# Kernel tuning notes

Hardware: AMD Instinct MI355X
Metric: run time of the kernel (lower is better)

The kernel has to match this reference:

```python
import jax, jax.numpy as jnp
import numpy as np

NUM_EXPERT = 8
TOP_K = 1


def setup_inputs() -> dict:
    key = jax.random.key(0)
    ks = jax.random.split(key, 6)
    B, S, D, E, F = 8, 2048, 768, 8, 469
    scale = 0.02
    return {
        "x": jax.random.normal(ks[0], (B, S, D), dtype=jnp.float32),
        "Wg": jax.random.normal(ks[1], (E, D), dtype=jnp.float32) * scale,
        "bg": jnp.zeros((E,), dtype=jnp.float32),
        "W1": jax.random.normal(ks[2], (E, F, D), dtype=jnp.float32) * scale,
        "W2": jax.random.normal(ks[3], (E, F, D), dtype=jnp.float32) * scale,
        "W3": jax.random.normal(ks[4], (E, D, F), dtype=jnp.float32) * scale,
    }


def reference(x, Wg, bg, W1, W2, W3):
    # x: [B, S, D]; Wg: [E, D]; W1/W2: [E, F, D] (torch Linear layout [out,in]); W3: [E, D, F]
    B, S, D = x.shape
    E = Wg.shape[0]
    xf = x.reshape(B * S, D)  # [T, D]

    # gating: top-k over expert logits, softmax over the selected logits
    gate = xf @ Wg.T + bg  # [T, E]
    vals, idx = jax.lax.top_k(gate, TOP_K)  # [T, K]
    probs = jax.nn.softmax(vals, axis=-1)  # [T, K] (all ones for K=1)

    # combine weights per (token, expert): sum over k slots of onehot * prob
    dispatch = jnp.sum(
        jax.nn.one_hot(idx, E, dtype=x.dtype) * probs[..., None], axis=1
    )  # [T, E]

    # dense grouped SwiGLU FFN over all experts, combined by dispatch weights
    h = jax.nn.silu(jnp.einsum("td,efd->tef", xf, W1)) * jnp.einsum(
        "td,efd->tef", xf, W2
    )  # [T, E, F]
    out = jnp.einsum("tef,edf,te->td", h, W3, dispatch)  # [T, D]
    return out.reshape(B, S, D)
```

## Files before the change

kernel.cpp:

```cpp
#include <hip/hip_runtime.h>
#include <hip/hip_bf16.h>
#include <stdint.h>

#define TT 16384
#define DD 768
#define EE 8
#define FF 469
#define FP 512
#define NCHUNK (TT / 64)
#define MAXT 71

typedef __attribute__((ext_vector_type(8))) short s16x8;
typedef __attribute__((ext_vector_type(4))) float f32x4;

__device__ __forceinline__ ushort f2bf(float f) {
  uint32_t u = __builtin_bit_cast(uint32_t, f);
  u += 0x7fffu + ((u >> 16) & 1u);
  return (ushort)(u >> 16);
}

__device__ __forceinline__ void gload16(const void* g, void* l) {
  __builtin_amdgcn_global_load_lds((const __attribute__((address_space(1))) unsigned int*)g,
                                   (__attribute__((address_space(3))) unsigned int*)l,
                                   16, 0, 0);
}

#define N12 (EE * 2 * FP * (DD / 4))
#define N3  (EE * DD * (FP / 4))
__global__ __launch_bounds__(256) void prep_kernel(
    const float* __restrict__ x, const float* __restrict__ Wg,
    const float* __restrict__ bg, const float* __restrict__ W1,
    const float* __restrict__ W2, const float* __restrict__ W3,
    int* __restrict__ eidx, ushort* __restrict__ xbf, int* __restrict__ cnt,
    ushort* __restrict__ w12b, ushort* __restrict__ w3b) {
  int tid = threadIdx.x;
  if (blockIdx.x < TT / 4) {
    __shared__ float4 wgs[EE * DD / 4];
    for (int i = tid; i < EE * DD / 4; i += 256) wgs[i] = ((const float4*)Wg)[i];
    __syncthreads();

    int t = blockIdx.x * 4 + (tid >> 6);
    int lane = tid & 63;
    const float4* xr = (const float4*)(x + (size_t)t * DD);
    float4 xv[3];
#pragma unroll
    for (int k = 0; k < 3; ++k) xv[k] = xr[lane + 64 * k];

    float acc[EE];
#pragma unroll
    for (int e = 0; e < EE; ++e) acc[e] = 0.f;
#pragma unroll
    for (int k = 0; k < 3; ++k) {
#pragma unroll
      for (int e = 0; e < EE; ++e) {
        float4 w = wgs[e * 192 + lane + 64 * k];
        acc[e] += xv[k].x * w.x + xv[k].y * w.y + xv[k].z * w.z + xv[k].w * w.w;
      }
    }

    uint2* xd = (uint2*)(xbf + (size_t)t * DD);
#pragma unroll
    for (int k = 0; k < 3; ++k) {
      union { ushort u[4]; uint2 w; } p;
      p.u[0] = f2bf(xv[k].x); p.u[1] = f2bf(xv[k].y);
      p.u[2] = f2bf(xv[k].z); p.u[3] = f2bf(xv[k].w);
      xd[lane + 64 * k] = p.w;
    }

#pragma unroll
    for (int off = 32; off; off >>= 1) {
#pragma unroll
      for (int e = 0; e < EE; ++e) acc[e] += __shfl_down(acc[e], off);
    }
    if (lane == 0) {
      float best = acc[0] + bg[0];
      int bi = 0;
#pragma unroll
      for (int e = 1; e < EE; ++e) {
        float v = acc[e] + bg[e];
        if (v > best) { best = v; bi = e; }
      }
      eidx[t] = bi;
      atomicAdd(&cnt[bi * NCHUNK + (t >> 6)], 1);
    }
  } else {
    int vb = blockIdx.x - TT / 4;
    for (int i = vb * 256 + tid; i < N12 + N3; i += 2048 * 256) {
      if (i < N12) {
        int d4 = i % (DD / 4);
        int er = i / (DD / 4);
        int row = er & 1023;
        int e = er >> 10;
        int f = row >> 1;
        union { ushort u[4]; uint2 w; } p;
        if (f < FF) {
          const float* src = ((row & 1) ? W2 : W1) + ((size_t)e * FF + f) * DD;
          float4 v = ((const float4*)src)[d4];
          p.u[0] = f2bf(v.x); p.u[1] = f2bf(v.y); p.u[2] = f2bf(v.z); p.u[3] = f2bf(v.w);
        } else {
          p.w.x = 0u; p.w.y = 0u;
        }
        ((uint2*)w12b)[i] = p.w;
      } else {
        int j = i - N12;
        int f4 = (j % (FP / 4)) * 4;
        int ed = j / (FP / 4);
        union { ushort u[4]; uint2 w; } p;
#pragma unroll
        for (int q = 0; q < 4; ++q) {
          int f = f4 + q;
          p.u[q] = (f < FF) ? f2bf(W3[(size_t)ed * FF + f]) : (ushort)0;
        }
        ((uint2*)w3b)[(size_t)ed * (FP / 4) + (f4 >> 2)] = p.w;
      }
    }
  }
}

__global__ void scan_kernel(const int* __restrict__ cnt, int* __restrict__ scanEx,
                            int* __restrict__ offs, int* __restrict__ tileE,
                            int* __restrict__ tileT0) {
  int e = threadIdx.x >> 6;
  int lane = threadIdx.x & 63;
  __shared__ int totals[EE];
  int carry = 0;
#pragma unroll
  for (int g = 0; g < NCHUNK / 64; ++g) {
    int v = cnt[e * NCHUNK + g * 64 + lane];
    int s = v;
#pragma unroll
    for (int d = 1; d < 64; d <<= 1) {
      int t = __shfl_up(s, d);
      if (lane >= d) s += t;
    }
    scanEx[e * NCHUNK + g * 64 + lane] = carry + s - v;
    carry += __shfl(s, 63);
  }
  if (lane == 0) totals[e] = carry;
  __syncthreads();
  if (threadIdx.x == 0) {
    int s = 0;
    for (int e2 = 0; e2 < EE; ++e2) { offs[e2] = s; s += totals[e2]; }
    offs[EE] = s;
    int idx = 0;
    for (int e2 = 0; e2 < EE; ++e2) {
      int nt = (totals[e2] + 255) >> 8;
      for (int j = 0; j < nt; ++j) { tileE[idx] = e2; tileT0[idx] = j << 8; ++idx; }
    }
    for (; idx < MAXT; ++idx) tileE[idx] = -1;
  }
}

__global__ void scatter2_kernel(const int* __restrict__ eidx, const int* __restrict__ offs,
                                const int* __restrict__ scanEx, int* __restrict__ perm) {
  int c = blockIdx.x * 4 + (threadIdx.x >> 6);
  int lane = threadIdx.x & 63;
  int t = c * 64 + lane;
  int v = eidx[t];
  unsigned long long mym = 0;
#pragma unroll
  for (int e = 0; e < EE; ++e) {
    unsigned long long me = __ballot(v == e);
    if (v == e) mym = me;
  }
  int rank = __popcll(mym & ((1ULL << lane) - 1ULL));
  perm[offs[v] + scanEx[v * NCHUNK + c] + rank] = t;
}

__global__ __launch_bounds__(512, 2) void ffn1_kernel(
    const ushort* __restrict__ xbf, const ushort* __restrict__ w12b,
    const int* __restrict__ perm, const int* __restrict__ offs,
    const int* __restrict__ tileE, const int* __restrict__ tileT0,
    ushort* __restrict__ hbf) {
  int bid = blockIdx.x;
  int xcd = bid & 7, idx = bid >> 3;
  int L = (xcd < 4) ? xcd * 36 + idx : 144 + (xcd - 4) * 35 + idx;
  int ti = L >> 2, y = L & 3;
  int e = tileE[ti];
  if (e < 0) return;
  int tile0 = tileT0[ti];
  int gOff = offs[e];
  int Ne = offs[e + 1] - gOff;
  int n0 = y * 256;

  __shared__ __align__(16) short As[2][256 * 64];
  __shared__ __align__(16) short Bs[2][256 * 64];

  int tid = threadIdx.x;
  int w = tid >> 6, lane = tid & 63;
  int l8 = lane >> 3, lg = lane & 7;
  int gsrc = (lg ^ l8) * 8;

  int last = gOff + Ne - 1;
  const ushort* aSrc[4];
  const ushort* bSrc[4];
#pragma unroll
  for (int j = 0; j < 4; ++j) {
    int row = w * 32 + j * 8 + l8;
    int tok = perm[min(gOff + tile0 + row, last)];
    aSrc[j] = xbf + (size_t)tok * DD + gsrc;
    bSrc[j] = w12b + ((size_t)(e << 10) + n0 + row) * DD + gsrc;
  }
  int sdst[4];
#pragma unroll
  for (int j = 0; j < 4; ++j) sdst[j] = (w * 32 + j * 8) * 64;

  int wr = w >> 2, wc = w & 3;
  int lrow = lane & 15, kh = lane >> 4;
  int sw0 = (kh ^ (lrow & 7)) * 8;
  int sw1 = ((4 + kh) ^ (lrow & 7)) * 8;
  int aBase = (wr * 128 + lrow) * 64;
  int bBase = (wc * 64 + lrow) * 64;

  f32x4 acc[2][2][4][2];
#pragma unroll
  for (int mh = 0; mh < 2; ++mh)
#pragma unroll
    for (int nh = 0; nh < 2; ++nh)
#pragma unroll
      for (int mm = 0; mm < 4; ++mm)
#pragma unroll
        for (int nn = 0; nn < 2; ++nn)
          acc[mh][nh][mm][nn] = (f32x4){0.f, 0.f, 0.f, 0.f};

#pragma unroll
  for (int j = 0; j < 4; ++j) gload16(aSrc[j], &As[0][sdst[j]]);
#pragma unroll
  for (int j = 0; j < 4; ++j) gload16(bSrc[j], &Bs[0][sdst[j]]);

  const int NT = DD / 64;
#pragma unroll
  for (int kt = 0; kt < NT; ++kt) {
    const int s = kt & 1;
    asm volatile("s_waitcnt vmcnt(0)" ::: "memory");
    __builtin_amdgcn_s_barrier();
    __builtin_amdgcn_sched_barrier(0);
    const int ko = (kt + 1) * 64;
    const bool more = (kt + 1 < NT);

    s16x8 a[4][2], b[2][2][2];
    if (more) {
      gload16(aSrc[0] + ko, &As[s ^ 1][sdst[0]]);
      gload16(aSrc[1] + ko, &As[s ^ 1][sdst[1]]);
    }
#pragma unroll
    for (int nh = 0; nh < 2; ++nh)
#pragma unroll
      for (int nn = 0; nn < 2; ++nn) {
        int rb = bBase + (nh * 32 + nn * 16) * 64;
        b[nh][nn][0] = *(const s16x8*)&Bs[s][rb + sw0];
        b[nh][nn][1] = *(const s16x8*)&Bs[s][rb + sw1];
      }
#pragma unroll
    for (int mm = 0; mm < 4; ++mm) {
      int ra = aBase + (mm * 16) * 64;
      a[mm][0] = *(const s16x8*)&As[s][ra + sw0];
      a[mm][1] = *(const s16x8*)&As[s][ra + sw1];
    }
    __builtin_amdgcn_s_setprio(1);
#pragma unroll
    for (int mm = 0; mm < 4; ++mm)
#pragma unroll
      for (int nn = 0; nn < 2; ++nn)
#pragma unroll
        for (int ks = 0; ks < 2; ++ks)
          acc[0][0][mm][nn] = __builtin_amdgcn_mfma_f32_16x16x32_bf16(a[mm][ks], b[0][nn][ks], acc[0][0][mm][nn], 0, 0, 0);
    __builtin_amdgcn_s_setprio(0);
    if (more) {
      gload16(aSrc[2] + ko, &As[s ^ 1][sdst[2]]);
      gload16(aSrc[3] + ko, &As[s ^ 1][sdst[3]]);
    }
    __builtin_amdgcn_s_setprio(1);
#pragma unroll
    for (int mm = 0; mm < 4; ++mm)
#pragma unroll
      for (int nn = 0; nn < 2; ++nn)
#pragma unroll
        for (int ks = 0; ks < 2; ++ks)
          acc[0][1][mm][nn] = __builtin_amdgcn_mfma_f32_16x16x32_bf16(a[mm][ks], b[1][nn][ks], acc[0][1][mm][nn], 0, 0, 0);
    __builtin_amdgcn_s_setprio(0);
    if (more) {
      gload16(bSrc[0] + ko, &Bs[s ^ 1][sdst[0]]);
      gload16(bSrc[1] + ko, &Bs[s ^ 1][sdst[1]]);
    }
#pragma unroll
    for (int mm = 0; mm < 4; ++mm) {
      int ra = aBase + (64 + mm * 16) * 64;
      a[mm][0] = *(const s16x8*)&As[s][ra + sw0];
      a[mm][1] = *(const s16x8*)&As[s][ra + sw1];
    }
    __builtin_amdgcn_s_setprio(1);
#pragma unroll
    for (int mm = 0; mm < 4; ++mm)
#pragma unroll
      for (int nn = 0; nn < 2; ++nn)
#pragma unroll
        for (int ks = 0; ks < 2; ++ks)
          acc[1][0][mm][nn] = __builtin_amdgcn_mfma_f32_16x16x32_bf16(a[mm][ks], b[0][nn][ks], acc[1][0][mm][nn], 0, 0, 0);
    __builtin_amdgcn_s_setprio(0);
    if (more) {
      gload16(bSrc[2] + ko, &Bs[s ^ 1][sdst[2]]);
      gload16(bSrc[3] + ko, &Bs[s ^ 1][sdst[3]]);
    }
    __builtin_amdgcn_s_setprio(1);
#pragma unroll
    for (int mm = 0; mm < 4; ++mm)
#pragma unroll
      for (int nn = 0; nn < 2; ++nn)
#pragma unroll
        for (int ks = 0; ks < 2; ++ks)
          acc[1][1][mm][nn] = __builtin_amdgcn_mfma_f32_16x16x32_bf16(a[mm][ks], b[1][nn][ks], acc[1][1][mm][nn], 0, 0, 0);
    __builtin_amdgcn_s_setprio(0);
  }

#pragma unroll
  for (int mh = 0; mh < 2; ++mh)
#pragma unroll
    for (int nh = 0; nh < 2; ++nh)
#pragma unroll
      for (int mm = 0; mm < 4; ++mm)
#pragma unroll
        for (int nn = 0; nn < 2; ++nn) {
          int f = (n0 + wc * 64 + nh * 32 + nn * 16 + lrow) >> 1;
          int rbase = tile0 + wr * 128 + mh * 64 + mm * 16 + kh * 4;
#pragma unroll
          for (int r = 0; r < 4; ++r) {
            float val = acc[mh][nh][mm][nn][r];
            float par = __shfl_xor(val, 1);
            float u = (lane & 1) ? par : val;
            float vv = (lane & 1) ? val : par;
            float h = (u / (1.f + __expf(-u))) * vv;
            int gr = rbase + r;
            if (!(lane & 1) && gr < Ne)
              hbf[(size_t)(gOff + gr) * FP + f] = f2bf(h);
          }
        }
}

__global__ __launch_bounds__(512, 2) void ffn2_kernel(
    const ushort* __restrict__ hbf, const ushort* __restrict__ w3b,
    const int* __restrict__ perm, const int* __restrict__ offs,
    const int* __restrict__ tileE, const int* __restrict__ tileT0,
    float* __restrict__ out) {
  int bid = blockIdx.x;
  int xcd = bid & 7, idx = bid >> 3;
  int L = (xcd < 5) ? xcd * 27 + idx : 135 + (xcd - 5) * 26 + idx;
  int ti = L / 3, y = L % 3;
  int e = tileE[ti];
  if (e < 0) return;
  int tile0 = tileT0[ti];
  int gOff = offs[e];
  int Ne = offs[e + 1] - gOff;
  int d0 = y * 256;

  __shared__ __align__(16) short As[2][256 * 64];
  __shared__ __align__(16) short Bs[2][256 * 64];

  int tid = threadIdx.x;
  int w = tid >> 6, lane = tid & 63;
  int l8 = lane >> 3, lg = lane & 7;
  int gsrc = (lg ^ l8) * 8;

  int last = gOff + Ne - 1;
  const ushort* aSrc[4];
  const ushort* bSrc[4];
#pragma unroll
  for (int j = 0; j < 4; ++j) {
    int row = w * 32 + j * 8 + l8;
    aSrc[j] = hbf + (size_t)min(gOff + tile0 + row, last) * FP + gsrc;
    bSrc[j] = w3b + ((size_t)e * DD + d0 + row) * FP + gsrc;
  }
  int sdst[4];
#pragma unroll
  for (int j = 0; j < 4; ++j) sdst[j] = (w * 32 + j * 8) * 64;

  int wr = w >> 2, wc = w & 3;
  int lrow = lane & 15, kh = lane >> 4;
  int sw0 = (kh ^ (lrow & 7)) * 8;
  int sw1 = ((4 + kh) ^ (lrow & 7)) * 8;
  int aBase = (wr * 128 + lrow) * 64;
  int bBase = (wc * 64 + lrow) * 64;

  f32x4 acc[2][2][4][2];
#pragma unroll
  for (int mh = 0; mh < 2; ++mh)
#pragma unroll
    for (int nh = 0; nh < 2; ++nh)
#pragma unroll
      for (int mm = 0; mm < 4; ++mm)
#pragma unroll
        for (int nn = 0; nn < 2; ++nn)
          acc[mh][nh][mm][nn] = (f32x4){0.f, 0.f, 0.f, 0.f};

#pragma unroll
  for (int j = 0; j < 4; ++j) gload16(aSrc[j], &As[0][sdst[j]]);
#pragma unroll
  for (int j = 0; j < 4; ++j) gload16(bSrc[j], &Bs[0][sdst[j]]);

  const int NT = FP / 64;
#pragma unroll
  for (int kt = 0; kt < NT; ++kt) {
    const int s = kt & 1;
    asm volatile("s_waitcnt vmcnt(0)" ::: "memory");
    __builtin_amdgcn_s_barrier();
    __builtin_amdgcn_sched_barrier(0);
    const int ko = (kt + 1) * 64;
    const bool more = (kt + 1 < NT);

    s16x8 a[4][2], b[2][2][2];
    if (more) {
      gload16(aSrc[0] + ko, &As[s ^ 1][sdst[0]]);
      gload16(aSrc[1] + ko, &As[s ^ 1][sdst[1]]);
    }
#pragma unroll
    for (int nh = 0; nh < 2; ++nh)
#pragma unroll
      for (int nn = 0; nn < 2; ++nn) {
        int rb = bBase + (nh * 32 + nn * 16) * 64;
        b[nh][nn][0] = *(const s16x8*)&Bs[s][rb + sw0];
        b[nh][nn][1] = *(const s16x8*)&Bs[s][rb + sw1];
      }
#pragma unroll
    for (int mm = 0; mm < 4; ++mm) {
      int ra = aBase + (mm * 16) * 64;
      a[mm][0] = *(const s16x8*)&As[s][ra + sw0];
      a[mm][1] = *(const s16x8*)&As[s][ra + sw1];
    }
    __builtin_amdgcn_s_setprio(1);
#pragma unroll
    for (int mm = 0; mm < 4; ++mm)
#pragma unroll
      for (int nn = 0; nn < 2; ++nn)
#pragma unroll
        for (int ks = 0; ks < 2; ++ks)
          acc[0][0][mm][nn] = __builtin_amdgcn_mfma_f32_16x16x32_bf16(a[mm][ks], b[0][nn][ks], acc[0][0][mm][nn], 0, 0, 0);
    __builtin_amdgcn_s_setprio(0);
    if (more) {
      gload16(aSrc[2] + ko, &As[s ^ 1][sdst[2]]);
      gload16(aSrc[3] + ko, &As[s ^ 1][sdst[3]]);
    }
    __builtin_amdgcn_s_setprio(1);
#pragma unroll
    for (int mm = 0; mm < 4; ++mm)
#pragma unroll
      for (int nn = 0; nn < 2; ++nn)
#pragma unroll
        for (int ks = 0; ks < 2; ++ks)
          acc[0][1][mm][nn] = __builtin_amdgcn_mfma_f32_16x16x32_bf16(a[mm][ks], b[1][nn][ks], acc[0][1][mm][nn], 0, 0, 0);
    __builtin_amdgcn_s_setprio(0);
    if (more) {
      gload16(bSrc[0] + ko, &Bs[s ^ 1][sdst[0]]);
      gload16(bSrc[1] + ko, &Bs[s ^ 1][sdst[1]]);
    }
#pragma unroll
    for (int mm = 0; mm < 4; ++mm) {
      int ra = aBase + (64 + mm * 16) * 64;
      a[mm][0] = *(const s16x8*)&As[s][ra + sw0];
      a[mm][1] = *(const s16x8*)&As[s][ra + sw1];
    }
    __builtin_amdgcn_s_setprio(1);
#pragma unroll
    for (int mm = 0; mm < 4; ++mm)
#pragma unroll
      for (int nn = 0; nn < 2; ++nn)
#pragma unroll
        for (int ks = 0; ks < 2; ++ks)
          acc[1][0][mm][nn] = __builtin_amdgcn_mfma_f32_16x16x32_bf16(a[mm][ks], b[0][nn][ks], acc[1][0][mm][nn], 0, 0, 0);
    __builtin_amdgcn_s_setprio(0);
    if (more) {
      gload16(bSrc[2] + ko, &Bs[s ^ 1][sdst[2]]);
      gload16(bSrc[3] + ko, &Bs[s ^ 1][sdst[3]]);
    }
    __builtin_amdgcn_s_setprio(1);
#pragma unroll
    for (int mm = 0; mm < 4; ++mm)
#pragma unroll
      for (int nn = 0; nn < 2; ++nn)
#pragma unroll
        for (int ks = 0; ks < 2; ++ks)
          acc[1][1][mm][nn] = __builtin_amdgcn_mfma_f32_16x16x32_bf16(a[mm][ks], b[1][nn][ks], acc[1][1][mm][nn], 0, 0, 0);
    __builtin_amdgcn_s_setprio(0);
  }

#pragma unroll
  for (int mh = 0; mh < 2; ++mh)
#pragma unroll
    for (int nh = 0; nh < 2; ++nh)
#pragma unroll
      for (int mm = 0; mm < 4; ++mm)
#pragma unroll
        for (int nn = 0; nn < 2; ++nn) {
          int col = d0 + wc * 64 + nh * 32 + nn * 16 + lrow;
          int rbase = tile0 + wr * 128 + mh * 64 + mm * 16 + kh * 4;
#pragma unroll
          for (int r = 0; r < 4; ++r) {
            int gr = rbase + r;
            if (gr < Ne) {
              int t = perm[gOff + gr];
              out[(size_t)t * DD + col] = acc[mh][nh][mm][nn][r];
            }
          }
        }
}

extern "C" void kernel_launch(void* const* d_in, const int* in_sizes, int n_in,
                              void* d_out, int out_size, void* d_ws, size_t ws_size,
                              hipStream_t stream) {
  const float* x = (const float*)d_in[0];
  const float* Wg = (const float*)d_in[1];
  const float* bg = (const float*)d_in[2];
  const float* W1 = (const float*)d_in[3];
  const float* W2 = (const float*)d_in[4];
  const float* W3 = (const float*)d_in[5];
  float* out = (float*)d_out;

  char* ws = (char*)d_ws;
  int* eidx = (int*)ws;
  int* perm = (int*)(ws + 65536);
  int* offs = (int*)(ws + 131072);
  int* cnt = (int*)(ws + 131072 + 128);
  int* scanEx = (int*)(ws + 131072 + 128 + 8192);
  int* tileE = (int*)(ws + 131072 + 128 + 16384);
  int* tileT0 = tileE + MAXT + 8;
  ushort* xbf = (ushort*)(ws + 262144);
  ushort* w12b = xbf + (size_t)TT * DD;
  ushort* w3b = w12b + (size_t)EE * 2 * FP * DD;
  ushort* hbf = w3b + (size_t)EE * DD * FP;

  hipMemsetAsync(cnt, 0, EE * NCHUNK * 4, stream);
  prep_kernel<<<TT / 4 + 2048, 256, 0, stream>>>(x, Wg, bg, W1, W2, W3,
                                                 eidx, xbf, cnt, w12b, w3b);
  scan_kernel<<<1, 512, 0, stream>>>(cnt, scanEx, offs, tileE, tileT0);
  scatter2_kernel<<<NCHUNK / 4, 256, 0, stream>>>(eidx, offs, scanEx, perm);
  ffn1_kernel<<<284, 512, 0, stream>>>(xbf, w12b, perm, offs, tileE, tileT0, hbf);
  ffn2_kernel<<<213, 512, 0, stream>>>(hbf, w3b, perm, offs, tileE, tileT0, out);
}
```

Measured before the change: 147.7 us.

## Restructure MoE GEMM mainloops into half-tile staged pipeline with partial vmcnt waits

Both grouped GEMM kernels now split the A and B shared-memory tiles into two 128-row halves. Loads are issued per half: B runs two k-steps ahead, A runs one ahead. Each stage waits with a partial vmcnt plus an explicit lgkmcnt and uses extra barriers between MFMA quarter-phases, so a buffer half can be refilled as soon as its readers are done. The goal is to hide global-to-LDS latency better than the single full vmcnt(0) wait per k-step. The cost is more barriers per iteration and tricky counter reasoning that could stall or race if the vmcnt values are off.

```diff
diff --git a/kernel.cpp b/kernel.cpp
--- a/kernel.cpp
+++ b/kernel.cpp
@@ -167,6 +167,7 @@
   perm[offs[v] + scanEx[v * NCHUNK + c] + rank] = t;
 }
 
+
 __global__ __launch_bounds__(512, 2) void ffn1_kernel(
     const ushort* __restrict__ xbf, const ushort* __restrict__ w12b,
     const int* __restrict__ perm, const int* __restrict__ offs,
@@ -183,34 +184,33 @@
   int Ne = offs[e + 1] - gOff;
   int n0 = y * 256;
 
-  __shared__ __align__(16) short As[2][256 * 64];
-  __shared__ __align__(16) short Bs[2][256 * 64];
+  __shared__ __align__(16) short As[2][2][128 * 64];
+  __shared__ __align__(16) short Bs[2][2][128 * 64];
 
   int tid = threadIdx.x;
   int w = tid >> 6, lane = tid & 63;
-  int l8 = lane >> 3, lg = lane & 7;
-  int gsrc = (lg ^ l8) * 8;
-
+  int gsrc = ((lane & 7) ^ ((lane >> 3) & 7)) * 8;
   int last = gOff + Ne - 1;
-  const ushort* aSrc[4];
-  const ushort* bSrc[4];
-#pragma unroll
-  for (int j = 0; j < 4; ++j) {
-    int row = w * 32 + j * 8 + l8;
-    int tok = perm[min(gOff + tile0 + row, last)];
-    aSrc[j] = xbf + (size_t)tok * DD + gsrc;
-    bSrc[j] = w12b + ((size_t)(e << 10) + n0 + row) * DD + gsrc;
-  }
-  int sdst[4];
-#pragma unroll
-  for (int j = 0; j < 4; ++j) sdst[j] = (w * 32 + j * 8) * 64;
+
+  const ushort* aS[2][2];
+  const ushort* bS[2][2];
+#pragma unroll
+  for (int h = 0; h < 2; ++h)
+#pragma unroll
+    for (int r = 0; r < 2; ++r) {
+      int row = h * 128 + r * 64 + w * 8 + (lane >> 3);
+      int tok = perm[min(gOff + tile0 + row, last)];
+      aS[h][r] = xbf + (size_t)tok * DD + gsrc;
+      bS[h][r] = w12b + ((size_t)(e << 10) + n0 + row) * DD + gsrc;
+    }
+  int ldst[2];
+  ldst[0] = w * 512;
+  ldst[1] = 4096 + w * 512;
 
   int wr = w >> 2, wc = w & 3;
   int lrow = lane & 15, kh = lane >> 4;
-  int sw0 = (kh ^ (lrow & 7)) * 8;
-  int sw1 = ((4 + kh) ^ (lrow & 7)) * 8;
-  int aBase = (wr * 128 + lrow) * 64;
-  int bBase = (wc * 64 + lrow) * 64;
+  int sw[2] = {((kh) ^ (lrow & 7)) * 8, ((4 + kh) ^ (lrow & 7)) * 8};
+  int bh = wc >> 1, brow0 = (wc & 1) * 64;
 
   f32x4 acc[2][2][4][2];
 #pragma unroll
@@ -224,39 +224,47 @@
           acc[mh][nh][mm][nn] = (f32x4){0.f, 0.f, 0.f, 0.f};
 
 #pragma unroll
-  for (int j = 0; j < 4; ++j) gload16(aSrc[j], &As[0][sdst[j]]);
-#pragma unroll
-  for (int j = 0; j < 4; ++j) gload16(bSrc[j], &Bs[0][sdst[j]]);
+  for (int h = 0; h < 2; ++h)
+#pragma unroll
+    for (int r = 0; r < 2; ++r) gload16(aS[h][r], &As[0][h][ldst[r]]);
+#pragma unroll
+  for (int h = 0; h < 2; ++h)
+#pragma unroll
+    for (int r = 0; r < 2; ++r) gload16(bS[h][r], &Bs[0][h][ldst[r]]);
+#pragma unroll
+  for (int h = 0; h < 2; ++h)
+#pragma unroll
+    for (int r = 0; r < 2; ++r) gload16(bS[h][r] + 64, &Bs[1][h][ldst[r]]);
 
   const int NT = DD / 64;
+  s16x8 a[4][2], b[2][2][2];
 #pragma unroll
   for (int kt = 0; kt < NT; ++kt) {
     const int s = kt & 1;
-    asm volatile("s_waitcnt vmcnt(0)" ::: "memory");
-    __builtin_amdgcn_s_barrier();
-    __builtin_amdgcn_sched_barrier(0);
-    const int ko = (kt + 1) * 64;
-    const bool more = (kt + 1 < NT);
-
-    s16x8 a[4][2], b[2][2][2];
-    if (more) {
-      gload16(aSrc[0] + ko, &As[s ^ 1][sdst[0]]);
-      gload16(aSrc[1] + ko, &As[s ^ 1][sdst[1]]);
-    }
-#pragma unroll
-    for (int nh = 0; nh < 2; ++nh)
-#pragma unroll
-      for (int nn = 0; nn < 2; ++nn) {
-        int rb = bBase + (nh * 32 + nn * 16) * 64;
-        b[nh][nn][0] = *(const s16x8*)&Bs[s][rb + sw0];
-        b[nh][nn][1] = *(const s16x8*)&Bs[s][rb + sw1];
-      }
+    const int kc = kt * 64;
+    if (kt + 1 < NT) {
+      gload16(aS[0][0] + kc + 64, &As[s ^ 1][0][ldst[0]]);
+      gload16(aS[0][1] + kc + 64, &As[s ^ 1][0][ldst[1]]);
+      asm volatile("s_waitcnt vmcnt(6)" ::: "memory");
+    } else {
+      asm volatile("s_waitcnt vmcnt(0)" ::: "memory");
+    }
+    __builtin_amdgcn_s_barrier();
+    __builtin_amdgcn_sched_barrier(0);
 #pragma unroll
     for (int mm = 0; mm < 4; ++mm) {
-      int ra = aBase + (mm * 16) * 64;
-      a[mm][0] = *(const s16x8*)&As[s][ra + sw0];
-      a[mm][1] = *(const s16x8*)&As[s][ra + sw1];
-    }
+      int ra = (mm * 16 + lrow) * 64;
+      a[mm][0] = *(const s16x8*)&As[s][wr][ra + sw[0]];
+      a[mm][1] = *(const s16x8*)&As[s][wr][ra + sw[1]];
+    }
+#pragma unroll
+    for (int nn = 0; nn < 2; ++nn) {
+      int rb = (brow0 + nn * 16 + lrow) * 64;
+      b[0][nn][0] = *(const s16x8*)&Bs[s][bh][rb + sw[0]];
+      b[0][nn][1] = *(const s16x8*)&Bs[s][bh][rb + sw[1]];
+    }
+    asm volatile("s_waitcnt lgkmcnt(0)" ::: "memory");
+    __builtin_amdgcn_sched_barrier(0);
     __builtin_amdgcn_s_setprio(1);
 #pragma unroll
     for (int mm = 0; mm < 4; ++mm)
@@ -266,10 +274,19 @@
         for (int ks = 0; ks < 2; ++ks)
           acc[0][0][mm][nn] = __builtin_amdgcn_mfma_f32_16x16x32_bf16(a[mm][ks], b[0][nn][ks], acc[0][0][mm][nn], 0, 0, 0);
     __builtin_amdgcn_s_setprio(0);
-    if (more) {
-      gload16(aSrc[2] + ko, &As[s ^ 1][sdst[2]]);
-      gload16(aSrc[3] + ko, &As[s ^ 1][sdst[3]]);
-    }
+    __builtin_amdgcn_s_barrier();
+#pragma unroll
+    for (int nn = 0; nn < 2; ++nn) {
+      int rb = (brow0 + 32 + nn * 16 + lrow) * 64;
+      b[1][nn][0] = *(const s16x8*)&Bs[s][bh][rb + sw[0]];
+      b[1][nn][1] = *(const s16x8*)&Bs[s][bh][rb + sw[1]];
+    }
+    if (kt + 1 < NT) {
+      gload16(aS[1][0] + kc + 64, &As[s ^ 1][1][ldst[0]]);
+      gload16(aS[1][1] + kc + 64, &As[s ^ 1][1][ldst[1]]);
+    }
+    asm volatile("s_waitcnt lgkmcnt(0)" ::: "memory");
+    __builtin_amdgcn_sched_barrier(0);
     __builtin_amdgcn_s_setprio(1);
 #pragma unroll
     for (int mm = 0; mm < 4; ++mm)
@@ -279,16 +296,19 @@
         for (int ks = 0; ks < 2; ++ks)
           acc[0][1][mm][nn] = __builtin_amdgcn_mfma_f32_16x16x32_bf16(a[mm][ks], b[1][nn][ks], acc[0][1][mm][nn], 0, 0, 0);
     __builtin_amdgcn_s_setprio(0);
-    if (more) {
-      gload16(bSrc[0] + ko, &Bs[s ^ 1][sdst[0]]);
-      gload16(bSrc[1] + ko, &Bs[s ^ 1][sdst[1]]);
-    }
+    __builtin_amdgcn_s_barrier();
 #pragma unroll
     for (int mm = 0; mm < 4; ++mm) {
-      int ra = aBase + (64 + mm * 16) * 64;
-      a[mm][0] = *(const s16x8*)&As[s][ra + sw0];
-      a[mm][1] = *(const s16x8*)&As[s][ra + sw1];
-    }
+      int ra = (64 + mm * 16 + lrow) * 64;
+      a[mm][0] = *(const s16x8*)&As[s][wr][ra + sw[0]];
+      a[mm][1] = *(const s16x8*)&As[s][wr][ra + sw[1]];
+    }
+    if (kt + 2 < NT) {
+      gload16(bS[0][0] + kc + 128, &Bs[s][0][ldst[0]]);
+      gload16(bS[0][1] + kc + 128, &Bs[s][0][ldst[1]]);
+    }
+    asm volatile("s_waitcnt lgkmcnt(0)" ::: "memory");
+    __builtin_amdgcn_sched_barrier(0);
     __builtin_amdgcn_s_setprio(1);
 #pragma unroll
     for (int mm = 0; mm < 4; ++mm)
@@ -298,9 +318,10 @@
         for (int ks = 0; ks < 2; ++ks)
           acc[1][0][mm][nn] = __builtin_amdgcn_mfma_f32_16x16x32_bf16(a[mm][ks], b[0][nn][ks], acc[1][0][mm][nn], 0, 0, 0);
     __builtin_amdgcn_s_setprio(0);
-    if (more) {
-      gload16(bSrc[2] + ko, &Bs[s ^ 1][sdst[2]]);
-      gload16(bSrc[3] + ko, &Bs[s ^ 1][sdst[3]]);
+    __builtin_amdgcn_s_barrier();
+    if (kt + 2 < NT) {
+      gload16(bS[1][0] + kc + 128, &Bs[s][1][ldst[0]]);
+      gload16(bS[1][1] + kc + 128, &Bs[s][1][ldst[1]]);
     }
     __builtin_amdgcn_s_setprio(1);
 #pragma unroll
@@ -311,6 +332,7 @@
         for (int ks = 0; ks < 2; ++ks)
           acc[1][1][mm][nn] = __builtin_amdgcn_mfma_f32_16x16x32_bf16(a[mm][ks], b[1][nn][ks], acc[1][1][mm][nn], 0, 0, 0);
     __builtin_amdgcn_s_setprio(0);
+    __builtin_amdgcn_s_barrier();
   }
 
 #pragma unroll
@@ -353,33 +375,32 @@
   int Ne = offs[e + 1] - gOff;
   int d0 = y * 256;
 
-  __shared__ __align__(16) short As[2][256 * 64];
-  __shared__ __align__(16) short Bs[2][256 * 64];
+  __shared__ __align__(16) short As[2][2][128 * 64];
+  __shared__ __align__(16) short Bs[2][2][128 * 64];
 
   int tid = threadIdx.x;
   int w = tid >> 6, lane = tid & 63;
-  int l8 = lane >> 3, lg = lane & 7;
-  int gsrc = (lg ^ l8) * 8;
-
+  int gsrc = ((lane & 7) ^ ((lane >> 3) & 7)) * 8;
   int last = gOff + Ne - 1;
-  const ushort* aSrc[4];
-  const ushort* bSrc[4];
-#pragma unroll
-  for (int j = 0; j < 4; ++j) {
-    int row = w * 32 + j * 8 + l8;
-    aSrc[j] = hbf + (size_t)min(gOff + tile0 + row, last) * FP + gsrc;
-    bSrc[j] = w3b + ((size_t)e * DD + d0 + row) * FP + gsrc;
-  }
-  int sdst[4];
-#pragma unroll
-  for (int j = 0; j < 4; ++j) sdst[j] = (w * 32 + j * 8) * 64;
+
+  const ushort* aS[2][2];
+  const ushort* bS[2][2];
+#pragma unroll
+  for (int h = 0; h < 2; ++h)
+#pragma unroll
+    for (int r = 0; r < 2; ++r) {
+      int row = h * 128 + r * 64 + w * 8 + (lane >> 3);
+      aS[h][r] = hbf + (size_t)min(gOff + tile0 + row, last) * FP + gsrc;
+      bS[h][r] = w3b + ((size_t)e * DD + d0 + row) * FP + gsrc;
+    }
+  int ldst[2];
+  ldst[0] = w * 512;
+  ldst[1] = 4096 + w * 512;
 
   int wr = w >> 2, wc = w & 3;
   int lrow = lane & 15, kh = lane >> 4;
-  int sw0 = (kh ^ (lrow & 7)) * 8;
-  int sw1 = ((4 + kh) ^ (lrow & 7)) * 8;
-  int aBase = (wr * 128 + lrow) * 64;
-  int bBase = (wc * 64 + lrow) * 64;
+  int sw[2] = {((kh) ^ (lrow & 7)) * 8, ((4 + kh) ^ (lrow & 7)) * 8};
+  int bh = wc >> 1, brow0 = (wc & 1) * 64;
 
   f32x4 acc[2][2][4][2];
 #pragma unroll
@@ -393,39 +414,47 @@
           acc[mh][nh][mm][nn] = (f32x4){0.f, 0.f, 0.f, 0.f};
 
 #pragma unroll
-  for (int j = 0; j < 4; ++j) gload16(aSrc[j], &As[0][sdst[j]]);
-#pragma unroll
-  for (int j = 0; j < 4; ++j) gload16(bSrc[j], &Bs[0][sdst[j]]);
+  for (int h = 0; h < 2; ++h)
+#pragma unroll
+    for (int r = 0; r < 2; ++r) gload16(aS[h][r], &As[0][h][ldst[r]]);
+#pragma unroll
+  for (int h = 0; h < 2; ++h)
+#pragma unroll
+    for (int r = 0; r < 2; ++r) gload16(bS[h][r], &Bs[0][h][ldst[r]]);
+#pragma unroll
+  for (int h = 0; h < 2; ++h)
+#pragma unroll
+    for (int r = 0; r < 2; ++r) gload16(bS[h][r] + 64, &Bs[1][h][ldst[r]]);
 
   const int NT = FP / 64;
+  s16x8 a[4][2], b[2][2][2];
 #pragma unroll
   for (int kt = 0; kt < NT; ++kt) {
     const int s = kt & 1;
-    asm volatile("s_waitcnt vmcnt(0)" ::: "memory");
-    __builtin_amdgcn_s_barrier();
-    __builtin_amdgcn_sched_barrier(0);
-    const int ko = (kt + 1) * 64;
-    const bool more = (kt + 1 < NT);
-
-    s16x8 a[4][2], b[2][2][2];
-    if (more) {
-      gload16(aSrc[0] + ko, &As[s ^ 1][sdst[0]]);
-      gload16(aSrc[1] + ko, &As[s ^ 1][sdst[1]]);
-    }
-#pragma unroll
-    for (int nh = 0; nh < 2; ++nh)
-#pragma unroll
-      for (int nn = 0; nn < 2; ++nn) {
-        int rb = bBase + (nh * 32 + nn * 16) * 64;
-        b[nh][nn][0] = *(const s16x8*)&Bs[s][rb + sw0];
-        b[nh][nn][1] = *(const s16x8*)&Bs[s][rb + sw1];
-      }
+    const int kc = kt * 64;
+    if (kt + 1 < NT) {
+      gload16(aS[0][0] + kc + 64, &As[s ^ 1][0][ldst[0]]);
+      gload16(aS[0][1] + kc + 64, &As[s ^ 1][0][ldst[1]]);
+      asm volatile("s_waitcnt vmcnt(6)" ::: "memory");
+    } else {
+      asm volatile("s_waitcnt vmcnt(0)" ::: "memory");
+    }
+    __builtin_amdgcn_s_barrier();
+    __builtin_amdgcn_sched_barrier(0);
 #pragma unroll
     for (int mm = 0; mm < 4; ++mm) {
-      int ra = aBase + (mm * 16) * 64;
-      a[mm][0] = *(const s16x8*)&As[s][ra + sw0];
-      a[mm][1] = *(const s16x8*)&As[s][ra + sw1];
-    }
+      int ra = (mm * 16 + lrow) * 64;
+      a[mm][0] = *(const s16x8*)&As[s][wr][ra + sw[0]];
+      a[mm][1] = *(const s16x8*)&As[s][wr][ra + sw[1]];
+    }
+#pragma unroll
+    for (int nn = 0; nn < 2; ++nn) {
+      int rb = (brow0 + nn * 16 + lrow) * 64;
+      b[0][nn][0] = *(const s16x8*)&Bs[s][bh][rb + sw[0]];
+      b[0][nn][1] = *(const s16x8*)&Bs[s][bh][rb + sw[1]];
+    }
+    asm volatile("s_waitcnt lgkmcnt(0)" ::: "memory");
+    __builtin_amdgcn_sched_barrier(0);
     __builtin_amdgcn_s_setprio(1);
 #pragma unroll
     for (int mm = 0; mm < 4; ++mm)
@@ -435,10 +464,19 @@
         for (int ks = 0; ks < 2; ++ks)
           acc[0][0][mm][nn] = __builtin_amdgcn_mfma_f32_16x16x32_bf16(a[mm][ks], b[0][nn][ks], acc[0][0][mm][nn], 0, 0, 0);
     __builtin_amdgcn_s_setprio(0);
-    if (more) {
-      gload16(aSrc[2] + ko, &As[s ^ 1][sdst[2]]);
-      gload16(aSrc[3] + ko, &As[s ^ 1][sdst[3]]);
-    }
+    __builtin_amdgcn_s_barrier();
+#pragma unroll
+    for (int nn = 0; nn < 2; ++nn) {
+      int rb = (brow0 + 32 + nn * 16 + lrow) * 64;
+      b[1][nn][0] = *(const s16x8*)&Bs[s][bh][rb + sw[0]];
+      b[1][nn][1] = *(const s16x8*)&Bs[s][bh][rb + sw[1]];
+    }
+    if (kt + 1 < NT) {
+      gload16(aS[1][0] + kc + 64, &As[s ^ 1][1][ldst[0]]);
+      gload16(aS[1][1] + kc + 64, &As[s ^ 1][1][ldst[1]]);
+    }
+    asm volatile("s_waitcnt lgkmcnt(0)" ::: "memory");
+    __builtin_amdgcn_sched_barrier(0);
     __builtin_amdgcn_s_setprio(1);
 #pragma unroll
     for (int mm = 0; mm < 4; ++mm)
@@ -448,16 +486,19 @@
         for (int ks = 0; ks < 2; ++ks)
           acc[0][1][mm][nn] = __builtin_amdgcn_mfma_f32_16x16x32_bf16(a[mm][ks], b[1][nn][ks], acc[0][1][mm][nn], 0, 0, 0);
     __builtin_amdgcn_s_setprio(0);
-    if (more) {
-      gload16(bSrc[0] + ko, &Bs[s ^ 1][sdst[0]]);
-      gload16(bSrc[1] + ko, &Bs[s ^ 1][sdst[1]]);
-    }
+    __builtin_amdgcn_s_barrier();
 #pragma unroll
     for (int mm = 0; mm < 4; ++mm) {
-      int ra = aBase + (64 + mm * 16) * 64;
-      a[mm][0] = *(const s16x8*)&As[s][ra + sw0];
-      a[mm][1] = *(const s16x8*)&As[s][ra + sw1];
-    }
+      int ra = (64 + mm * 16 + lrow) * 64;
+      a[mm][0] = *(const s16x8*)&As[s][wr][ra + sw[0]];
+      a[mm][1] = *(const s16x8*)&As[s][wr][ra + sw[1]];
+    }
+    if (kt + 2 < NT) {
+      gload16(bS[0][0] + kc + 128, &Bs[s][0][ldst[0]]);
+      gload16(bS[0][1] + kc + 128, &Bs[s][0][ldst[1]]);
+    }
+    asm volatile("s_waitcnt lgkmcnt(0)" ::: "memory");
+    __builtin_amdgcn_sched_barrier(0);
     __builtin_amdgcn_s_setprio(1);
 #pragma unroll
     for (int mm = 0; mm < 4; ++mm)
@@ -467,9 +508,10 @@
         for (int ks = 0; ks < 2; ++ks)
           acc[1][0][mm][nn] = __builtin_amdgcn_mfma_f32_16x16x32_bf16(a[mm][ks], b[0][nn][ks], acc[1][0][mm][nn], 0, 0, 0);
     __builtin_amdgcn_s_setprio(0);
-    if (more) {
-      gload16(bSrc[2] + ko, &Bs[s ^ 1][sdst[2]]);
-      gload16(bSrc[3] + ko, &Bs[s ^ 1][sdst[3]]);
+    __builtin_amdgcn_s_barrier();
+    if (kt + 2 < NT) {
+      gload16(bS[1][0] + kc + 128, &Bs[s][1][ldst[0]]);
+      gload16(bS[1][1] + kc + 128, &Bs[s][1][ldst[1]]);
     }
     __builtin_amdgcn_s_setprio(1);
 #pragma unroll
@@ -480,6 +522,7 @@
         for (int ks = 0; ks < 2; ++ks)
           acc[1][1][mm][nn] = __builtin_amdgcn_mfma_f32_16x16x32_bf16(a[mm][ks], b[1][nn][ks], acc[1][1][mm][nn], 0, 0, 0);
     __builtin_amdgcn_s_setprio(0);
+    __builtin_amdgcn_s_barrier();
   }
 
 #pragma unroll
```

Measured after the change: 141.8 us. 1.04x faster.
